# Kernel tuning notes

Measured on AMD Instinct MI355X. Metric: run time of the kernel, lower is better.

The kernel has to match this reference:

```python
import jax, jax.numpy as jnp
import numpy as np

N_NODES = 100000
N_EDGES = 3200000
IN_CH = 128
HID_CH = 64
NEG_SLOPE = 0.2  # PyG GATConv default leaky_relu slope


def setup_inputs() -> dict:
    key = jax.random.key(0)
    k1, k2, k3, k4, k5, k6 = jax.random.split(key, 6)
    x = jax.random.normal(k1, (N_NODES, IN_CH), dtype=jnp.float32)
    edge_index = jax.random.randint(k2, (2, N_EDGES), 0, N_NODES, dtype=jnp.int64)
    # learned params of GATConv(in, hid, heads=1)
    W = jax.random.normal(k3, (IN_CH, HID_CH), dtype=jnp.float32) / np.sqrt(IN_CH)
    att_src = jax.random.normal(k4, (HID_CH,), dtype=jnp.float32) / np.sqrt(HID_CH)
    att_dst = jax.random.normal(k5, (HID_CH,), dtype=jnp.float32) / np.sqrt(HID_CH)
    bias = jax.random.normal(k6, (HID_CH,), dtype=jnp.float32) * 0.01
    return {"x": x, "edge_index": edge_index, "W": W, "att_src": att_src,
            "att_dst": att_dst, "bias": bias}


def reference(x, edge_index, W, att_src, att_dst, bias):
    N = x.shape[0]
    h = x @ W  # [N, H] linear transform
    # PyG GATConv default: add self loops
    loops = jnp.arange(N, dtype=edge_index.dtype)
    src = jnp.concatenate([edge_index[0], loops])  # [E+N]
    dst = jnp.concatenate([edge_index[1], loops])
    # per-node attention halves, then gather per-edge
    a_src = h @ att_src  # [N]
    a_dst = h @ att_dst  # [N]
    e = jax.nn.leaky_relu(a_src[src] + a_dst[dst], NEG_SLOPE)  # [E+N]
    # segment softmax over incoming edges of each destination node
    m = jax.ops.segment_max(e, dst, num_segments=N)
    e = jnp.exp(e - m[dst])
    s = jax.ops.segment_sum(e, dst, num_segments=N)
    alpha = e / s[dst]  # [E+N]
    # scatter-aggregate weighted source features
    out = jax.ops.segment_sum(h[src] * alpha[:, None], dst, num_segments=N) + bias
    return out, alpha[:, None]
```

## Files before the change

kernel.cpp:

```cpp
#include <hip/hip_runtime.h>
#include <hip/hip_bf16.h>

#define IN_CH 128
#define HID 64
#define NEG_SLOPE 0.2f
#define BSH 9
#define CAP 18432

typedef __attribute__((ext_vector_type(8))) short short8;
typedef __attribute__((ext_vector_type(4))) float floatx4;

__device__ inline short bfr(float f) {
    unsigned u = __float_as_uint(f);
    u += 0x7fffu + ((u >> 16) & 1u);
    return (short)(u >> 16);
}

__global__ void k_prep(const float* __restrict__ W, short* __restrict__ wfrag,
                       int* __restrict__ g_cursor)
{
    if (blockIdx.x == 0) g_cursor[threadIdx.x] = 0;
    int idx = blockIdx.x * 256 + threadIdx.x;
    if (idx >= 1024) return;
    int f = idx >> 6, l = idx & 63;
    int kt = f >> 2, nt = f & 3;
    int k0 = kt * 32 + (l >> 4) * 8;
    int n = nt * 16 + (l & 15);
#pragma unroll
    for (int j = 0; j < 8; ++j)
        wfrag[idx * 8 + j] = bfr(W[(k0 + j) * HID + n]);
}

__global__ __launch_bounds__(256) void k_gemm(
    const float* __restrict__ x, const short8* __restrict__ wfrag,
    const float* __restrict__ att_src, const float* __restrict__ att_dst,
    short* __restrict__ h, float* __restrict__ a_src,
    float* __restrict__ a_dst, int N)
{
    const int t = threadIdx.x;
    const int lane = t & 63;
    const int wv = t >> 6;
    const int l15 = lane & 15;
    const int quad = lane >> 4;

    short8 bf[16];
#pragma unroll
    for (int f = 0; f < 16; ++f) bf[f] = wfrag[f * 64 + lane];

    float as4[4], ad4[4];
#pragma unroll
    for (int nt = 0; nt < 4; ++nt) {
        as4[nt] = att_src[nt * 16 + l15];
        ad4[nt] = att_dst[nt * 16 + l15];
    }

    const int rowbase = blockIdx.x * 128 + wv * 32;

#pragma unroll
    for (int mt = 0; mt < 2; ++mt) {
        const int m0 = rowbase + mt * 16;
        const int rowa = m0 + l15;
        const int rowc = rowa < N ? rowa : N - 1;
        const float* xp = x + (size_t)rowc * IN_CH + quad * 8;

        short8 af[4];
#pragma unroll
        for (int kt = 0; kt < 4; ++kt) {
            float4 p0 = *(const float4*)(xp + kt * 32);
            float4 p1 = *(const float4*)(xp + kt * 32 + 4);
            short8 a;
            a[0] = bfr(p0.x); a[1] = bfr(p0.y); a[2] = bfr(p0.z); a[3] = bfr(p0.w);
            a[4] = bfr(p1.x); a[5] = bfr(p1.y); a[6] = bfr(p1.z); a[7] = bfr(p1.w);
            af[kt] = a;
        }

        floatx4 acc[4];
#pragma unroll
        for (int nt = 0; nt < 4; ++nt) acc[nt] = (floatx4){0.f, 0.f, 0.f, 0.f};
#pragma unroll
        for (int kt = 0; kt < 4; ++kt)
#pragma unroll
            for (int nt = 0; nt < 4; ++nt)
                acc[nt] = __builtin_amdgcn_mfma_f32_16x16x32_bf16(
                    af[kt], bf[kt * 4 + nt], acc[nt], 0, 0, 0);

#pragma unroll
        for (int r = 0; r < 4; ++r) {
            const int row = m0 + quad * 4 + r;
            const bool ok = row < N;
            if (ok) {
#pragma unroll
                for (int nt = 0; nt < 4; ++nt)
                    h[(size_t)row * HID + nt * 16 + l15] = bfr(acc[nt][r]);
            }
            float ps = acc[0][r] * as4[0] + acc[1][r] * as4[1] +
                       acc[2][r] * as4[2] + acc[3][r] * as4[3];
            float pd = acc[0][r] * ad4[0] + acc[1][r] * ad4[1] +
                       acc[2][r] * ad4[2] + acc[3][r] * ad4[3];
#pragma unroll
            for (int m2 = 1; m2 < 16; m2 <<= 1) {
                ps += __shfl_xor(ps, m2, 64);
                pd += __shfl_xor(pd, m2, 64);
            }
            if (ok && l15 == 0) { a_src[row] = ps; a_dst[row] = pd; }
        }
    }
}

__global__ __launch_bounds__(256) void k_binB(
    const int* __restrict__ ei, int* __restrict__ g_cursor,
    int* __restrict__ pairs, int E, int nb)
{
    __shared__ int hist[256];
    __shared__ int base[256];
    const int t = threadIdx.x;
    hist[t] = 0;
    __syncthreads();

    int s[16], d[16];
    const int4* s4 = (const int4*)ei;
    const int4* d4 = (const int4*)(ei + E);
    const int E4 = E >> 2;
    const int q0 = blockIdx.x * 1024;
#pragma unroll
    for (int i = 0; i < 4; ++i) {
        int q = q0 + i * 256 + t;
        int4 sv = make_int4(0, 0, 0, 0);
        int4 dv = make_int4(-1, -1, -1, -1);
        if (q < E4) { sv = s4[q]; dv = d4[q]; }
        s[4 * i + 0] = sv.x; s[4 * i + 1] = sv.y; s[4 * i + 2] = sv.z; s[4 * i + 3] = sv.w;
        d[4 * i + 0] = dv.x; d[4 * i + 1] = dv.y; d[4 * i + 2] = dv.z; d[4 * i + 3] = dv.w;
    }
#pragma unroll
    for (int i = 0; i < 16; ++i)
        if (d[i] >= 0) atomicAdd(&hist[d[i] >> BSH], 1);
    __syncthreads();

    if (t < nb) base[t] = atomicAdd(&g_cursor[t], hist[t]);
    __syncthreads();
    hist[t] = 0;
    __syncthreads();

#pragma unroll
    for (int i = 0; i < 16; ++i) {
        if (d[i] < 0) continue;
        int b = d[i] >> BSH;
        int l = atomicAdd(&hist[b], 1);
        int pos = base[b] + l;
        if (pos < CAP)
            pairs[b * CAP + pos] = s[i] | ((d[i] & 511) << 17);
    }
}

__global__ __launch_bounds__(512) void k_binC(
    const int* __restrict__ pairs, const int* __restrict__ g_cursor,
    int* __restrict__ row_start, int* __restrict__ cnt,
    int* __restrict__ csr_src, int N, int nb)
{
    __shared__ int h0[512];
    __shared__ int hs[512];
    __shared__ int cur[512];
    __shared__ int sbase;
    const int t = threadIdx.x;
    const int b = blockIdx.x;
    const int d0 = b << BSH;
    const int m = g_cursor[b];
    const int* pb = pairs + b * CAP;

    int bv = (t < nb) ? g_cursor[t] : 0;
    hs[t] = bv;
    __syncthreads();
    for (int off = 1; off < 512; off <<= 1) {
        int u = (t >= off) ? hs[t - off] : 0;
        __syncthreads();
        hs[t] += u;
        __syncthreads();
    }
    if (t == b) sbase = hs[t] - bv;
    h0[t] = 0;
    __syncthreads();
    const int basec = sbase;

    for (int i = t; i < m; i += 512)
        atomicAdd(&h0[pb[i] >> 17], 1);
    __syncthreads();

    hs[t] = h0[t];
    __syncthreads();
    for (int off = 1; off < 512; off <<= 1) {
        int u = (t >= off) ? hs[t - off] : 0;
        __syncthreads();
        hs[t] += u;
        __syncthreads();
    }
    const int excl = hs[t] - h0[t];
    cur[t] = basec + excl;
    const int dd = d0 + t;
    if (dd < N) { row_start[dd] = basec + excl; cnt[dd] = h0[t]; }
    __syncthreads();

    for (int i = t; i < m; i += 512) {
        int p = pb[i];
        int pos = atomicAdd(&cur[p >> 17], 1);
        csr_src[pos] = p & 0x1FFFF;
    }
}

__global__ __launch_bounds__(256) void k_agg(
    const __hip_bfloat16* __restrict__ h, const float* __restrict__ a_src,
    const float* __restrict__ a_dst, const float* __restrict__ bias,
    const int* __restrict__ row_start, const int* __restrict__ cnt,
    const int* __restrict__ csr_src,
    float* __restrict__ out, float2* __restrict__ adi, int N)
{
    __shared__ float red[4][2][576];
    const int wave = threadIdx.x >> 6;
    const int lane = threadIdx.x & 63;
    const int d0 = blockIdx.x * 8 + wave * 2;
    if (d0 >= N) return;
    const int d1 = d0 + 1;
    const bool has1 = d1 < N;

    const int q  = lane >> 3;
    const int i8 = lane & 7;

    const float ad0 = a_dst[d0];
    const float ad1 = has1 ? a_dst[d1] : 0.f;
    const int st0 = row_start[d0];
    const int n0  = cnt[d0];
    const int en0 = st0 + n0;
    const int st1 = has1 ? row_start[d1] : 0;
    const int n1  = has1 ? cnt[d1] : 0;
    const int en1 = st1 + n1;

    const uint4* h4 = (const uint4*)h;

    float ps0 = 0.f, ps1 = 0.f;
    float ac0[8], ac1[8];
#pragma unroll
    for (int c = 0; c < 8; ++c) { ac0[c] = 0.f; ac1[c] = 0.f; }

    const int nbt0 = (n0 + 63) >> 6;
    const int nbt1 = (n1 + 63) >> 6;
    const int nbm = nbt0 > nbt1 ? nbt0 : nbt1;

    int b0 = st0, b1 = st1;
    for (int it = 0; it < nbm; ++it, b0 += 64, b1 += 64) {
        int s0v = 0, s1v = 0;
        float e0 = 0.f, e1 = 0.f;
        const int idx0 = b0 + lane;
        if (it < nbt0 && idx0 < en0) {
            s0v = csr_src[idx0];
            float v = a_src[s0v] + ad0;
            v = v > 0.f ? v : NEG_SLOPE * v;
            e0 = __expf(v);
            ps0 += e0;
        }
        const int idx1 = b1 + lane;
        if (it < nbt1 && idx1 < en1) {
            s1v = csr_src[idx1];
            float v = a_src[s1v] + ad1;
            v = v > 0.f ? v : NEG_SLOPE * v;
            e1 = __expf(v);
            ps1 += e1;
        }
        const int m0 = (it < nbt0) ? min(64, en0 - b0) : 0;
        const int m1 = (it < nbt1) ? min(64, en1 - b1) : 0;
        const int mm = m0 > m1 ? m0 : m1;
#pragma unroll 4
        for (int j = 0; j < mm; j += 8) {
            const int jq = j + q;
            const int sj0 = __shfl(s0v, jq, 64);
            const float ej0 = __shfl(e0, jq, 64);
            const int sj1 = __shfl(s1v, jq, 64);
            const float ej1 = __shfl(e1, jq, 64);
            uint4 u0 = h4[(size_t)sj0 * 8 + i8];
            uint4 u1 = h4[(size_t)sj1 * 8 + i8];
            ac0[0] = fmaf(ej0, __uint_as_float(u0.x << 16),         ac0[0]);
            ac0[1] = fmaf(ej0, __uint_as_float(u0.x & 0xffff0000u), ac0[1]);
            ac0[2] = fmaf(ej0, __uint_as_float(u0.y << 16),         ac0[2]);
            ac0[3] = fmaf(ej0, __uint_as_float(u0.y & 0xffff0000u), ac0[3]);
            ac0[4] = fmaf(ej0, __uint_as_float(u0.z << 16),         ac0[4]);
            ac0[5] = fmaf(ej0, __uint_as_float(u0.z & 0xffff0000u), ac0[5]);
            ac0[6] = fmaf(ej0, __uint_as_float(u0.w << 16),         ac0[6]);
            ac0[7] = fmaf(ej0, __uint_as_float(u0.w & 0xffff0000u), ac0[7]);
            ac1[0] = fmaf(ej1, __uint_as_float(u1.x << 16),         ac1[0]);
            ac1[1] = fmaf(ej1, __uint_as_float(u1.x & 0xffff0000u), ac1[1]);
            ac1[2] = fmaf(ej1, __uint_as_float(u1.y << 16),         ac1[2]);
            ac1[3] = fmaf(ej1, __uint_as_float(u1.y & 0xffff0000u), ac1[3]);
            ac1[4] = fmaf(ej1, __uint_as_float(u1.z << 16),         ac1[4]);
            ac1[5] = fmaf(ej1, __uint_as_float(u1.z & 0xffff0000u), ac1[5]);
            ac1[6] = fmaf(ej1, __uint_as_float(u1.w << 16),         ac1[6]);
            ac1[7] = fmaf(ej1, __uint_as_float(u1.w & 0xffff0000u), ac1[7]);
        }
    }

    float* r0 = &red[wave][0][0];
    float* r1 = &red[wave][1][0];
#pragma unroll
    for (int c = 0; c < 8; ++c) r0[lane * 9 + c] = ac0[c];
#pragma unroll
    for (int c = 0; c < 8; ++c) r1[lane * 9 + c] = ac1[c];

#pragma unroll
    for (int m2 = 32; m2 > 0; m2 >>= 1) {
        ps0 += __shfl_xor(ps0, m2, 64);
        ps1 += __shfl_xor(ps1, m2, 64);
    }

    float vs0 = a_src[d0] + ad0;
    vs0 = vs0 > 0.f ? vs0 : NEG_SLOPE * vs0;
    const float es0 = __expf(vs0);
    const float inv0 = 1.f / (ps0 + es0);
    float es1 = 0.f, inv1 = 0.f;
    if (has1) {
        float vs1 = a_src[d1] + ad1;
        vs1 = vs1 > 0.f ? vs1 : NEG_SLOPE * vs1;
        es1 = __expf(vs1);
        inv1 = 1.f / (ps1 + es1);
    }
    if (lane == 0) {
        adi[d0] = make_float2(ad0, inv0);
        if (has1) adi[d1] = make_float2(ad1, inv1);
    }

    const int oi = lane >> 3, oc = lane & 7;
    float s0 = 0.f, s1 = 0.f;
#pragma unroll
    for (int qq = 0; qq < 8; ++qq) {
        s0 += r0[(qq * 8 + oi) * 9 + oc];
        s1 += r1[(qq * 8 + oi) * 9 + oc];
    }

    const ushort* hu = (const ushort*)h;
    const float bi = bias[lane];
    float hs0 = __uint_as_float(((unsigned)hu[(size_t)d0 * HID + lane]) << 16);
    out[(size_t)d0 * HID + lane] = fmaf(es0, hs0, s0) * inv0 + bi;
    if (has1) {
        float hs1 = __uint_as_float(((unsigned)hu[(size_t)d1 * HID + lane]) << 16);
        out[(size_t)d1 * HID + lane] = fmaf(es1, hs1, s1) * inv1 + bi;
    }
}

__global__ void k_alpha(const int* __restrict__ ei,
                        const float* __restrict__ a_src,
                        const float2* __restrict__ adi,
                        float* __restrict__ out_alpha, int E, int N)
{
    int e = blockIdx.x * 256 + threadIdx.x;
    if (e >= E + N) return;
    int s, d;
    if (e < E) { s = ei[e]; d = ei[E + e]; }
    else       { s = e - E; d = s; }
    float2 av = adi[d];
    float v = a_src[s] + av.x;
    v = v > 0.f ? v : NEG_SLOPE * v;
    out_alpha[e] = __expf(v) * av.y;
}

extern "C" void kernel_launch(void* const* d_in, const int* in_sizes, int n_in,
                              void* d_out, int out_size, void* d_ws, size_t ws_size,
                              hipStream_t stream)
{
    (void)n_in; (void)out_size; (void)ws_size;
    const float* x       = (const float*)d_in[0];
    const int*   ei      = (const int*)d_in[1];
    const float* W       = (const float*)d_in[2];
    const float* att_src = (const float*)d_in[3];
    const float* att_dst = (const float*)d_in[4];
    const float* bias    = (const float*)d_in[5];

    const int N = in_sizes[0] / IN_CH;
    const int E = in_sizes[1] / 2;
    const int T = E + N;
    const int nb = (N + 511) >> BSH;

    __hip_bfloat16* h = (__hip_bfloat16*)d_ws;
    float* a_src_d = (float*)(h + (size_t)N * HID);
    float* a_dst_d = a_src_d + N;
    float2* adi    = (float2*)(a_dst_d + N);
    int* row_start = (int*)(adi + N);
    int* cnt       = row_start + N;
    int* g_cursor  = cnt + N;
    short* wfrag   = (short*)(g_cursor + 256);
    int* pairs     = (int*)(wfrag + 8192);
    int* csr_src   = pairs + (size_t)nb * CAP;

    float* out       = (float*)d_out;
    float* out_alpha = out + (size_t)N * HID;

    k_prep<<<4, 256, 0, stream>>>(W, wfrag, g_cursor);
    k_gemm<<<(N + 127) / 128, 256, 0, stream>>>(x, (const short8*)wfrag,
                                                att_src, att_dst,
                                                (short*)h, a_src_d, a_dst_d, N);
    k_binB<<<(E / 4 + 1023) / 1024, 256, 0, stream>>>(ei, g_cursor, pairs, E, nb);
    k_binC<<<nb, 512, 0, stream>>>(pairs, g_cursor,
                                   row_start, cnt, csr_src, N, nb);
    k_agg<<<(N + 7) / 8, 256, 0, stream>>>(h, a_src_d, a_dst_d, bias,
                                           row_start, cnt, csr_src,
                                           out, adi, N);
    k_alpha<<<(T + 255) / 256, 256, 0, stream>>>(ei, a_src_d, adi,
                                                 out_alpha, E, N);
}
```

Baseline: 273.3 us.

## Use smaller destination bins and stage edge weights in LDS for aggregation

```diff
diff --git a/kernel.cpp b/kernel.cpp
--- a/kernel.cpp
+++ b/kernel.cpp
@@ -4,11 +4,12 @@
 #define IN_CH 128
 #define HID 64
 #define NEG_SLOPE 0.2f
-#define BSH 9
-#define CAP 18432
+#define BSH 8
+#define CAP 10240
 
 typedef __attribute__((ext_vector_type(8))) short short8;
 typedef __attribute__((ext_vector_type(4))) float floatx4;
+typedef __attribute__((ext_vector_type(2))) float f32x2;
 
 __device__ inline short bfr(float f) {
     unsigned u = __float_as_uint(f);
@@ -19,7 +20,10 @@
 __global__ void k_prep(const float* __restrict__ W, short* __restrict__ wfrag,
                        int* __restrict__ g_cursor)
 {
-    if (blockIdx.x == 0) g_cursor[threadIdx.x] = 0;
+    if (blockIdx.x == 0) {
+        g_cursor[threadIdx.x] = 0;
+        g_cursor[threadIdx.x + 256] = 0;
+    }
     int idx = blockIdx.x * 256 + threadIdx.x;
     if (idx >= 1024) return;
     int f = idx >> 6, l = idx & 63;
@@ -111,10 +115,11 @@
     const int* __restrict__ ei, int* __restrict__ g_cursor,
     int* __restrict__ pairs, int E, int nb)
 {
-    __shared__ int hist[256];
-    __shared__ int base[256];
+    __shared__ int hist[512];
+    __shared__ int base[512];
     const int t = threadIdx.x;
     hist[t] = 0;
+    hist[t + 256] = 0;
     __syncthreads();
 
     int s[16], d[16];
@@ -137,8 +142,10 @@
     __syncthreads();
 
     if (t < nb) base[t] = atomicAdd(&g_cursor[t], hist[t]);
+    if (t + 256 < nb) base[t + 256] = atomicAdd(&g_cursor[t + 256], hist[t + 256]);
     __syncthreads();
     hist[t] = 0;
+    hist[t + 256] = 0;
     __syncthreads();
 
 #pragma unroll
@@ -148,7 +155,7 @@
         int l = atomicAdd(&hist[b], 1);
         int pos = base[b] + l;
         if (pos < CAP)
-            pairs[b * CAP + pos] = s[i] | ((d[i] & 511) << 17);
+            pairs[b * CAP + pos] = s[i] | ((d[i] & 255) << 17);
     }
 }
 
@@ -157,9 +164,9 @@
     int* __restrict__ row_start, int* __restrict__ cnt,
     int* __restrict__ csr_src, int N, int nb)
 {
-    __shared__ int h0[512];
+    __shared__ int h0[256];
     __shared__ int hs[512];
-    __shared__ int cur[512];
+    __shared__ int cur[256];
     __shared__ int sbase;
     const int t = threadIdx.x;
     const int b = blockIdx.x;
@@ -177,7 +184,7 @@
         __syncthreads();
     }
     if (t == b) sbase = hs[t] - bv;
-    h0[t] = 0;
+    if (t < 256) h0[t] = 0;
     __syncthreads();
     const int basec = sbase;
 
@@ -185,18 +192,20 @@
         atomicAdd(&h0[pb[i] >> 17], 1);
     __syncthreads();
 
-    hs[t] = h0[t];
-    __syncthreads();
-    for (int off = 1; off < 512; off <<= 1) {
-        int u = (t >= off) ? hs[t - off] : 0;
+    if (t < 256) hs[t] = h0[t];
+    __syncthreads();
+    for (int off = 1; off < 256; off <<= 1) {
+        int u = (t >= off && t < 256) ? hs[t - off] : 0;
         __syncthreads();
-        hs[t] += u;
+        if (t < 256) hs[t] += u;
         __syncthreads();
     }
-    const int excl = hs[t] - h0[t];
-    cur[t] = basec + excl;
-    const int dd = d0 + t;
-    if (dd < N) { row_start[dd] = basec + excl; cnt[dd] = h0[t]; }
+    if (t < 256) {
+        const int excl = hs[t] - h0[t];
+        cur[t] = basec + excl;
+        const int dd = d0 + t;
+        if (dd < N) { row_start[dd] = basec + excl; cnt[dd] = h0[t]; }
+    }
     __syncthreads();
 
     for (int i = t; i < m; i += 512) {
@@ -213,7 +222,9 @@
     const int* __restrict__ csr_src,
     float* __restrict__ out, float2* __restrict__ adi, int N)
 {
+    __shared__ uint2 se[4][2][64];
     __shared__ float red[4][2][576];
+
     const int wave = threadIdx.x >> 6;
     const int lane = threadIdx.x & 63;
     const int d0 = blockIdx.x * 8 + wave * 2;
@@ -224,25 +235,33 @@
     const int q  = lane >> 3;
     const int i8 = lane & 7;
 
-    const float ad0 = a_dst[d0];
-    const float ad1 = has1 ? a_dst[d1] : 0.f;
+    const float2 ad2 = *(const float2*)(a_dst + d0);
+    const float ad0 = ad2.x;
+    const float ad1 = ad2.y;
+    const int2 cn2 = *(const int2*)(cnt + d0);
+    const int n0 = cn2.x;
+    const int n1 = has1 ? cn2.y : 0;
     const int st0 = row_start[d0];
-    const int n0  = cnt[d0];
     const int en0 = st0 + n0;
-    const int st1 = has1 ? row_start[d1] : 0;
-    const int n1  = has1 ? cnt[d1] : 0;
+    const int st1 = en0;
     const int en1 = st1 + n1;
 
     const uint4* h4 = (const uint4*)h;
 
     float ps0 = 0.f, ps1 = 0.f;
-    float ac0[8], ac1[8];
-#pragma unroll
-    for (int c = 0; c < 8; ++c) { ac0[c] = 0.f; ac1[c] = 0.f; }
+    f32x2 ac0[4], ac1[4];
+#pragma unroll
+    for (int c = 0; c < 4; ++c) {
+        ac0[c] = (f32x2){0.f, 0.f};
+        ac1[c] = (f32x2){0.f, 0.f};
+    }
 
     const int nbt0 = (n0 + 63) >> 6;
     const int nbt1 = (n1 + 63) >> 6;
     const int nbm = nbt0 > nbt1 ? nbt0 : nbt1;
+
+    uint2* t0 = &se[wave][0][0];
+    uint2* t1 = &se[wave][1][0];
 
     int b0 = st0, b1 = st1;
     for (int it = 0; it < nbm; ++it, b0 += 64, b1 += 64) {
@@ -264,43 +283,59 @@
             e1 = __expf(v);
             ps1 += e1;
         }
+        t0[lane] = make_uint2((unsigned)s0v, __float_as_uint(e0));
+        t1[lane] = make_uint2((unsigned)s1v, __float_as_uint(e1));
+
         const int m0 = (it < nbt0) ? min(64, en0 - b0) : 0;
         const int m1 = (it < nbt1) ? min(64, en1 - b1) : 0;
         const int mm = m0 > m1 ? m0 : m1;
-#pragma unroll 4
+#pragma unroll 8
         for (int j = 0; j < mm; j += 8) {
-            const int jq = j + q;
-            const int sj0 = __shfl(s0v, jq, 64);
-            const float ej0 = __shfl(e0, jq, 64);
-            const int sj1 = __shfl(s1v, jq, 64);
-            const float ej1 = __shfl(e1, jq, 64);
-            uint4 u0 = h4[(size_t)sj0 * 8 + i8];
-            uint4 u1 = h4[(size_t)sj1 * 8 + i8];
-            ac0[0] = fmaf(ej0, __uint_as_float(u0.x << 16),         ac0[0]);
-            ac0[1] = fmaf(ej0, __uint_as_float(u0.x & 0xffff0000u), ac0[1]);
-            ac0[2] = fmaf(ej0, __uint_as_float(u0.y << 16),         ac0[2]);
-            ac0[3] = fmaf(ej0, __uint_as_float(u0.y & 0xffff0000u), ac0[3]);
-            ac0[4] = fmaf(ej0, __uint_as_float(u0.z << 16),         ac0[4]);
-            ac0[5] = fmaf(ej0, __uint_as_float(u0.z & 0xffff0000u), ac0[5]);
-            ac0[6] = fmaf(ej0, __uint_as_float(u0.w << 16),         ac0[6]);
-            ac0[7] = fmaf(ej0, __uint_as_float(u0.w & 0xffff0000u), ac0[7]);
-            ac1[0] = fmaf(ej1, __uint_as_float(u1.x << 16),         ac1[0]);
-            ac1[1] = fmaf(ej1, __uint_as_float(u1.x & 0xffff0000u), ac1[1]);
-            ac1[2] = fmaf(ej1, __uint_as_float(u1.y << 16),         ac1[2]);
-            ac1[3] = fmaf(ej1, __uint_as_float(u1.y & 0xffff0000u), ac1[3]);
-            ac1[4] = fmaf(ej1, __uint_as_float(u1.z << 16),         ac1[4]);
-            ac1[5] = fmaf(ej1, __uint_as_float(u1.z & 0xffff0000u), ac1[5]);
-            ac1[6] = fmaf(ej1, __uint_as_float(u1.w << 16),         ac1[6]);
-            ac1[7] = fmaf(ej1, __uint_as_float(u1.w & 0xffff0000u), ac1[7]);
+            const uint2 p0 = t0[j + q];
+            const uint2 p1 = t1[j + q];
+            const float ej0 = __uint_as_float(p0.y);
+            const float ej1 = __uint_as_float(p1.y);
+            uint4 u0 = h4[(size_t)p0.x * 8 + i8];
+            uint4 u1 = h4[(size_t)p1.x * 8 + i8];
+            f32x2 ev0; ev0[0] = ej0; ev0[1] = ej0;
+            f32x2 ev1; ev1[0] = ej1; ev1[1] = ej1;
+            f32x2 c;
+            c[0] = __uint_as_float(u0.x << 16);
+            c[1] = __uint_as_float(u0.x & 0xffff0000u);
+            ac0[0] = __builtin_elementwise_fma(ev0, c, ac0[0]);
+            c[0] = __uint_as_float(u0.y << 16);
+            c[1] = __uint_as_float(u0.y & 0xffff0000u);
+            ac0[1] = __builtin_elementwise_fma(ev0, c, ac0[1]);
+            c[0] = __uint_as_float(u0.z << 16);
+            c[1] = __uint_as_float(u0.z & 0xffff0000u);
+            ac0[2] = __builtin_elementwise_fma(ev0, c, ac0[2]);
+            c[0] = __uint_as_float(u0.w << 16);
+            c[1] = __uint_as_float(u0.w & 0xffff0000u);
+            ac0[3] = __builtin_elementwise_fma(ev0, c, ac0[3]);
+            c[0] = __uint_as_float(u1.x << 16);
+            c[1] = __uint_as_float(u1.x & 0xffff0000u);
+            ac1[0] = __builtin_elementwise_fma(ev1, c, ac1[0]);
+            c[0] = __uint_as_float(u1.y << 16);
+            c[1] = __uint_as_float(u1.y & 0xffff0000u);
+            ac1[1] = __builtin_elementwise_fma(ev1, c, ac1[1]);
+            c[0] = __uint_as_float(u1.z << 16);
+            c[1] = __uint_as_float(u1.z & 0xffff0000u);
+            ac1[2] = __builtin_elementwise_fma(ev1, c, ac1[2]);
+            c[0] = __uint_as_float(u1.w << 16);
+            c[1] = __uint_as_float(u1.w & 0xffff0000u);
+            ac1[3] = __builtin_elementwise_fma(ev1, c, ac1[3]);
         }
     }
 
     float* r0 = &red[wave][0][0];
     float* r1 = &red[wave][1][0];
 #pragma unroll
-    for (int c = 0; c < 8; ++c) r0[lane * 9 + c] = ac0[c];
-#pragma unroll
-    for (int c = 0; c < 8; ++c) r1[lane * 9 + c] = ac1[c];
+    for (int p = 0; p < 4; ++p) {
+        r0[lane * 9 + 2 * p]     = ac0[p][0];
+        r0[lane * 9 + 2 * p + 1] = ac0[p][1];
+        r1[lane * 9 + 2 * p]     = ac1[p][0];
+        r1[lane * 9 + 2 * p + 1] = ac1[p][1];
+    }
 
 #pragma unroll
     for (int m2 = 32; m2 > 0; m2 >>= 1) {
@@ -308,13 +343,14 @@
         ps1 += __shfl_xor(ps1, m2, 64);
     }
 
-    float vs0 = a_src[d0] + ad0;
+    const float2 asd = *(const float2*)(a_src + d0);
+    float vs0 = asd.x + ad0;
     vs0 = vs0 > 0.f ? vs0 : NEG_SLOPE * vs0;
     const float es0 = __expf(vs0);
     const float inv0 = 1.f / (ps0 + es0);
     float es1 = 0.f, inv1 = 0.f;
     if (has1) {
-        float vs1 = a_src[d1] + ad1;
+        float vs1 = asd.y + ad1;
         vs1 = vs1 > 0.f ? vs1 : NEG_SLOPE * vs1;
         es1 = __expf(vs1);
         inv1 = 1.f / (ps1 + es1);
@@ -373,7 +409,7 @@
     const int N = in_sizes[0] / IN_CH;
     const int E = in_sizes[1] / 2;
     const int T = E + N;
-    const int nb = (N + 511) >> BSH;
+    const int nb = (N + 255) >> BSH;
 
     __hip_bfloat16* h = (__hip_bfloat16*)d_ws;
     float* a_src_d = (float*)(h + (size_t)N * HID);
@@ -382,7 +418,7 @@
     int* row_start = (int*)(adi + N);
     int* cnt       = row_start + N;
     int* g_cursor  = cnt + N;
-    short* wfrag   = (short*)(g_cursor + 256);
+    short* wfrag   = (short*)(g_cursor + 512);
     int* pairs     = (int*)(wfrag + 8192);
     int* csr_src   = pairs + (size_t)nb * CAP;
 
```

Result: slower. 292.7 us (+7.1%).
